# Kernel optimization log

Measured on AMD Instinct MI355X. Metric: run time of the kernel, lower is better.

The kernel has to match this reference:

```python
import jax, jax.numpy as jnp
import numpy as np

N, F_IN, F_OUT = 32768, 1024, 512
ALPHA = 0.1  # leaky relu slope


def setup_inputs() -> dict:
    key = jax.random.key(0)
    k1, k2, k3, k4, k5 = jax.random.split(key, 5)
    h = jax.random.normal(k1, (1, F_IN), dtype=jnp.float32)
    adj = jax.random.uniform(k2, (N, F_IN), dtype=jnp.float32)
    # xavier-uniform-ish init for W and a, randn for W_1 (matches torch init flavor)
    limW = float(np.sqrt(6.0 / (F_IN + F_OUT)))
    W = jax.random.uniform(k3, (F_IN, F_OUT), minval=-limW, maxval=limW, dtype=jnp.float32)
    lima = float(np.sqrt(6.0 / (2 * F_OUT + 1)))
    a = jax.random.uniform(k4, (2 * F_OUT, 1), minval=-lima, maxval=lima, dtype=jnp.float32)
    W_1 = jax.random.normal(k5, (F_IN, F_OUT), dtype=jnp.float32)
    return {"h": h, "adj": adj, "W": W, "a": a, "W_1": W_1}


def reference(h, adj, W, a, W_1):
    # W_h: [1, Fo]; W_adj: [N, Fo]
    W_h = h @ W
    W_adj = adj @ W
    # Original: cat([W_h.repeat(N,1), W_adj], dim=1) @ a.
    # Equivalent additive decomposition: (W_h @ a1) + (W_adj @ a2) -> no [N, 2Fo] intermediate.
    Fo = W.shape[1]
    a1, a2 = a[:Fo], a[Fo:]
    scores = jax.nn.leaky_relu(W_h @ a1 + W_adj @ a2, negative_slope=ALPHA).squeeze(-1)  # [N]
    attention = jax.nn.softmax(scores)  # softmax over all N rows
    W_adj_transform = adj @ W_1  # [N, Fo]
    out = attention @ W_adj_transform  # [Fo]
    # attention2 in the source: 1 where attention > mean else 0 (as an int mask)
    attention2 = (attention > attention.mean()).astype(jnp.int32)
    return out, attention2
```

## Files before the change

### kernel.cpp

```cpp
#include <hip/hip_runtime.h>

static constexpr int NROWS = 32768;
static constexpr int FIN   = 1024;
static constexpr int FOUT  = 512;
static constexpr int NREP  = 16;


__global__ __launch_bounds__(256) void k1_prep(const float* __restrict__ W,
                                               const float* __restrict__ a,
                                               const float* __restrict__ h,
                                               float* __restrict__ v,
                                               double* __restrict__ hpart,
                                               float* __restrict__ u16) {
    if (blockIdx.x < 16) {
        ((float4*)u16)[blockIdx.x * 256 + threadIdx.x] =
            make_float4(0.f, 0.f, 0.f, 0.f);
    }

    const int k    = (blockIdx.x * blockDim.x + threadIdx.x) >> 6;
    const int lane = threadIdx.x & 63;

    const float4* Wrow = (const float4*)(W + (size_t)k * FOUT);
    float4 w0 = Wrow[lane];
    float4 w1 = Wrow[64 + lane];

    const float4* a4 = (const float4*)a;
    float4 a1_0 = a4[lane];
    float4 a1_1 = a4[64 + lane];
    float4 a2_0 = a4[128 + lane];
    float4 a2_1 = a4[192 + lane];

    double d1 = (double)w0.x * a1_0.x + (double)w0.y * a1_0.y +
                (double)w0.z * a1_0.z + (double)w0.w * a1_0.w +
                (double)w1.x * a1_1.x + (double)w1.y * a1_1.y +
                (double)w1.z * a1_1.z + (double)w1.w * a1_1.w;
    double d2 = (double)w0.x * a2_0.x + (double)w0.y * a2_0.y +
                (double)w0.z * a2_0.z + (double)w0.w * a2_0.w +
                (double)w1.x * a2_1.x + (double)w1.y * a2_1.y +
                (double)w1.z * a2_1.z + (double)w1.w * a2_1.w;

    #pragma unroll
    for (int off = 32; off; off >>= 1) {
        d1 += __shfl_xor(d1, off);
        d2 += __shfl_xor(d2, off);
    }
    if (lane == 0) {
        v[k]     = (float)d2;
        hpart[k] = (double)h[k] * d1;
    }
}

__global__ __launch_bounds__(256) void k2_main(const float* __restrict__ adj,
                                               const float* __restrict__ v,
                                               const double* __restrict__ hpart,
                                               double* __restrict__ e,
                                               float* __restrict__ u16,
                                               double* __restrict__ zpart) {
    __shared__ float  uls[4][1024];
    __shared__ double zls[4];

    const int wave  = threadIdx.x >> 6;
    const int lane  = threadIdx.x & 63;
    const int gwave = blockIdx.x * 4 + wave;

    double c0 = 0.0;
    #pragma unroll
    for (int j = 0; j < 16; ++j) c0 += hpart[j * 64 + lane];
    #pragma unroll
    for (int off = 32; off; off >>= 1) c0 += __shfl_xor(c0, off);

    const float4* v4 = (const float4*)v;
    float4 vf[4];
    #pragma unroll
    for (int q = 0; q < 4; ++q) vf[q] = v4[q * 64 + lane];

    float  uacc[4][4] = {};
    double zacc = 0.0;

    const int row0 = gwave * 8;
    for (int r = 0; r < 8; ++r) {
        const int row = row0 + r;
        const float4* arow = (const float4*)(adj + (size_t)row * FIN);
        float4 d[4];
        #pragma unroll
        for (int q = 0; q < 4; ++q) d[q] = arow[q * 64 + lane];

        double dot = 0.0;
        #pragma unroll
        for (int q = 0; q < 4; ++q) {
            dot += (double)d[q].x * vf[q].x + (double)d[q].y * vf[q].y +
                   (double)d[q].z * vf[q].z + (double)d[q].w * vf[q].w;
        }
        #pragma unroll
        for (int off = 32; off; off >>= 1) dot += __shfl_xor(dot, off);

        double s = c0 + dot;
        if (s < 0.0) s *= 0.1;
        const double ev = exp(s);
        zacc += ev;
        if (lane == 0) e[row] = ev;

        const float evf = (float)ev;
        #pragma unroll
        for (int q = 0; q < 4; ++q) {
            uacc[q][0] += evf * d[q].x;
            uacc[q][1] += evf * d[q].y;
            uacc[q][2] += evf * d[q].z;
            uacc[q][3] += evf * d[q].w;
        }
    }

    float4* uls4w = (float4*)&uls[wave][0];
    #pragma unroll
    for (int q = 0; q < 4; ++q)
        uls4w[q * 64 + lane] = make_float4(uacc[q][0], uacc[q][1], uacc[q][2], uacc[q][3]);

    if (lane == 0) zls[wave] = zacc;

    __syncthreads();

    const int t = threadIdx.x;
    const float4* uls4 = (const float4*)uls;
    float4 s0 = uls4[t];
    float4 s1 = uls4[256 + t];
    float4 s2 = uls4[512 + t];
    float4 s3 = uls4[768 + t];

    float* urep = u16 + (size_t)(blockIdx.x & (NREP - 1)) * 1024 + 4 * t;
    unsafeAtomicAdd(&urep[0], s0.x + s1.x + s2.x + s3.x);
    unsafeAtomicAdd(&urep[1], s0.y + s1.y + s2.y + s3.y);
    unsafeAtomicAdd(&urep[2], s0.z + s1.z + s2.z + s3.z);
    unsafeAtomicAdd(&urep[3], s0.w + s1.w + s2.w + s3.w);

    if (t == 0) zpart[blockIdx.x] = zls[0] + zls[1] + zls[2] + zls[3];
}

__device__ __forceinline__ double block_reduce_Z(const double* __restrict__ zpart,
                                                 double* zs) {
    const int t = threadIdx.x;
    zs[t] = zpart[t] + zpart[256 + t] + zpart[512 + t] + zpart[768 + t];
    __syncthreads();
    for (int st = 128; st > 0; st >>= 1) {
        if (t < st) zs[t] += zs[t + st];
        __syncthreads();
    }
    double Z = zs[0];
    __syncthreads();
    return Z;
}

__global__ __launch_bounds__(256) void k3_final(const double* __restrict__ e,
                                                const double* __restrict__ zpart,
                                                const float* __restrict__ u16,
                                                const float* __restrict__ W1,
                                                float* __restrict__ out) {
    __shared__ double zs[256];
    const double Z = block_reduce_Z(zpart, zs);
    const int t = threadIdx.x;

    if (blockIdx.x < 16) {
        __shared__ float us[1024];
        __shared__ float red[8][32];

        #pragma unroll
        for (int g = 0; g < 4; ++g) {
            const int k = g * 256 + t;
            float s = 0.f;
            #pragma unroll
            for (int rep = 0; rep < NREP; ++rep) s += u16[rep * 1024 + k];
            us[k] = s;
        }
        __syncthreads();

        const int cl  = t & 31;
        const int kg  = t >> 5;
        const int col = blockIdx.x * 32 + cl;
        float acc = 0.f;
        #pragma unroll 4
        for (int kk = 0; kk < 128; ++kk) {
            const int k = kg * 128 + kk;
            acc += us[k] * W1[(size_t)k * FOUT + col];
        }
        red[kg][cl] = acc;
        __syncthreads();
        if (t < 32) {
            float tot = 0.f;
            #pragma unroll
            for (int g = 0; g < 8; ++g) tot += red[g][t];
            out[blockIdx.x * 32 + t] = (float)((double)tot / Z);
        }
    } else {
        const int i = (blockIdx.x - 16) * 256 + t;
        out[FOUT + i] = (e[i] * (double)NROWS > Z) ? 1.0f : 0.0f;
    }
}

extern "C" void kernel_launch(void* const* d_in, const int* in_sizes, int n_in,
                              void* d_out, int out_size, void* d_ws, size_t ws_size,
                              hipStream_t stream) {
    const float* h   = (const float*)d_in[0];
    const float* adj = (const float*)d_in[1];
    const float* W   = (const float*)d_in[2];
    const float* a   = (const float*)d_in[3];
    const float* W1  = (const float*)d_in[4];
    float* out = (float*)d_out;

    double* e     = (double*)d_ws;
    double* hpart = e + NROWS;
    double* zpart = hpart + 1024;
    float*  v     = (float*)(zpart + 1024);
    float*  u16   = v + 1024;

    k1_prep<<<dim3(256),  dim3(256), 0, stream>>>(W, a, h, v, hpart, u16);
    k2_main<<<dim3(1024), dim3(256), 0, stream>>>(adj, v, hpart, e, u16, zpart);
    k3_final<<<dim3(144), dim3(256), 0, stream>>>(e, zpart, u16, W1, out);
}
```

Before: 225.5 us.

## Split fused score/aggregation kernel into two passes with batched row loads

The single pass over adj is split into two kernels. The first computes scores, exp values and partial Z, batching 4 rows per iteration so loads and shuffle reductions overlap. The second re-reads adj to accumulate the e-weighted row sums, handling two rows per iteration. This aims to shorten the serial load-reduce-exp dependency chain and raise memory-level parallelism, at the cost of reading the 128 MB adj matrix twice plus one extra launch.

New measurement: 249.2 us. +10.5%, slower.

```diff
diff --git a/kernel.cpp b/kernel.cpp
--- a/kernel.cpp
+++ b/kernel.cpp
@@ -50,13 +50,11 @@
     }
 }
 
-__global__ __launch_bounds__(256) void k2_main(const float* __restrict__ adj,
-                                               const float* __restrict__ v,
-                                               const double* __restrict__ hpart,
-                                               double* __restrict__ e,
-                                               float* __restrict__ u16,
-                                               double* __restrict__ zpart) {
-    __shared__ float  uls[4][1024];
+__global__ __launch_bounds__(256) void k2a_scores(const float* __restrict__ adj,
+                                                  const float* __restrict__ v,
+                                                  const double* __restrict__ hpart,
+                                                  double* __restrict__ e,
+                                                  double* __restrict__ zpart) {
     __shared__ double zls[4];
 
     const int wave  = threadIdx.x >> 6;
@@ -74,39 +72,98 @@
     #pragma unroll
     for (int q = 0; q < 4; ++q) vf[q] = v4[q * 64 + lane];
 
-    float  uacc[4][4] = {};
     double zacc = 0.0;
-
     const int row0 = gwave * 8;
-    for (int r = 0; r < 8; ++r) {
-        const int row = row0 + r;
-        const float4* arow = (const float4*)(adj + (size_t)row * FIN);
-        float4 d[4];
-        #pragma unroll
-        for (int q = 0; q < 4; ++q) d[q] = arow[q * 64 + lane];
-
-        double dot = 0.0;
+
+    #pragma unroll
+    for (int b = 0; b < 2; ++b) {
+        const int r0 = row0 + b * 4;
+
+        float4 d[4][4];
+        #pragma unroll
+        for (int r = 0; r < 4; ++r) {
+            const float4* arow = (const float4*)(adj + (size_t)(r0 + r) * FIN);
+            #pragma unroll
+            for (int q = 0; q < 4; ++q) d[r][q] = arow[q * 64 + lane];
+        }
+
+        double dot[4];
+        #pragma unroll
+        for (int r = 0; r < 4; ++r) {
+            double t = 0.0;
+            #pragma unroll
+            for (int q = 0; q < 4; ++q) {
+                t += (double)d[r][q].x * vf[q].x + (double)d[r][q].y * vf[q].y +
+                     (double)d[r][q].z * vf[q].z + (double)d[r][q].w * vf[q].w;
+            }
+            dot[r] = t;
+        }
+
+        #pragma unroll
+        for (int off = 32; off; off >>= 1) {
+            #pragma unroll
+            for (int r = 0; r < 4; ++r) dot[r] += __shfl_xor(dot[r], off);
+        }
+
+        double ev[4];
+        #pragma unroll
+        for (int r = 0; r < 4; ++r) {
+            double s = c0 + dot[r];
+            if (s < 0.0) s *= 0.1;
+            ev[r] = exp(s);
+            zacc += ev[r];
+        }
+        if (lane == 0) {
+            e[r0 + 0] = ev[0];
+            e[r0 + 1] = ev[1];
+            e[r0 + 2] = ev[2];
+            e[r0 + 3] = ev[3];
+        }
+    }
+
+    if (lane == 0) zls[wave] = zacc;
+    __syncthreads();
+    if (threadIdx.x == 0) zpart[blockIdx.x] = zls[0] + zls[1] + zls[2] + zls[3];
+}
+
+__global__ __launch_bounds__(256) void k2b_u(const float* __restrict__ adj,
+                                             const double* __restrict__ e,
+                                             float* __restrict__ u16) {
+    __shared__ float uls[4][1024];
+
+    const int wave  = threadIdx.x >> 6;
+    const int lane  = threadIdx.x & 63;
+    const int gwave = blockIdx.x * 4 + wave;
+    const int row0  = gwave * 8;
+
+    float uacc[4][4] = {};
+
+    #pragma unroll
+    for (int r = 0; r < 8; r += 2) {
+        const float4* arow0 = (const float4*)(adj + (size_t)(row0 + r) * FIN);
+        const float4* arow1 = (const float4*)(adj + (size_t)(row0 + r + 1) * FIN);
+        float4 d0[4], d1[4];
+        #pragma unroll
+        for (int q = 0; q < 4; ++q) d0[q] = arow0[q * 64 + lane];
+        #pragma unroll
+        for (int q = 0; q < 4; ++q) d1[q] = arow1[q * 64 + lane];
+
+        const float e0 = (float)e[row0 + r];
+        const float e1 = (float)e[row0 + r + 1];
+
         #pragma unroll
         for (int q = 0; q < 4; ++q) {
-            dot += (double)d[q].x * vf[q].x + (double)d[q].y * vf[q].y +
-                   (double)d[q].z * vf[q].z + (double)d[q].w * vf[q].w;
-        }
-        #pragma unroll
-        for (int off = 32; off; off >>= 1) dot += __shfl_xor(dot, off);
-
-        double s = c0 + dot;
-        if (s < 0.0) s *= 0.1;
-        const double ev = exp(s);
-        zacc += ev;
-        if (lane == 0) e[row] = ev;
-
-        const float evf = (float)ev;
+            uacc[q][0] += e0 * d0[q].x;
+            uacc[q][1] += e0 * d0[q].y;
+            uacc[q][2] += e0 * d0[q].z;
+            uacc[q][3] += e0 * d0[q].w;
+        }
         #pragma unroll
         for (int q = 0; q < 4; ++q) {
-            uacc[q][0] += evf * d[q].x;
-            uacc[q][1] += evf * d[q].y;
-            uacc[q][2] += evf * d[q].z;
-            uacc[q][3] += evf * d[q].w;
+            uacc[q][0] += e1 * d1[q].x;
+            uacc[q][1] += e1 * d1[q].y;
+            uacc[q][2] += e1 * d1[q].z;
+            uacc[q][3] += e1 * d1[q].w;
         }
     }
 
@@ -114,8 +171,6 @@
     #pragma unroll
     for (int q = 0; q < 4; ++q)
         uls4w[q * 64 + lane] = make_float4(uacc[q][0], uacc[q][1], uacc[q][2], uacc[q][3]);
-
-    if (lane == 0) zls[wave] = zacc;
 
     __syncthreads();
 
@@ -131,8 +186,6 @@
     unsafeAtomicAdd(&urep[1], s0.y + s1.y + s2.y + s3.y);
     unsafeAtomicAdd(&urep[2], s0.z + s1.z + s2.z + s3.z);
     unsafeAtomicAdd(&urep[3], s0.w + s1.w + s2.w + s3.w);
-
-    if (t == 0) zpart[blockIdx.x] = zls[0] + zls[1] + zls[2] + zls[3];
 }
 
 __device__ __forceinline__ double block_reduce_Z(const double* __restrict__ zpart,
@@ -211,7 +264,8 @@
     float*  v     = (float*)(zpart + 1024);
     float*  u16   = v + 1024;
 
-    k1_prep<<<dim3(256),  dim3(256), 0, stream>>>(W, a, h, v, hpart, u16);
-    k2_main<<<dim3(1024), dim3(256), 0, stream>>>(adj, v, hpart, e, u16, zpart);
-    k3_final<<<dim3(144), dim3(256), 0, stream>>>(e, zpart, u16, W1, out);
-}
+    k1_prep<<<dim3(256),    dim3(256), 0, stream>>>(W, a, h, v, hpart, u16);
+    k2a_scores<<<dim3(1024), dim3(256), 0, stream>>>(adj, v, hpart, e, zpart);
+    k2b_u<<<dim3(1024),     dim3(256), 0, stream>>>(adj, e, u16);
+    k3_final<<<dim3(144),   dim3(256), 0, stream>>>(e, zpart, u16, W1, out);
+}
```
